# Kernel tuning notes

Hardware: AMD Instinct MI355X
Metric: run time of the kernel (lower is better)

## Reference

```python
import jax, jax.numpy as jnp
import numpy as np

B, S, HID, NH, CACHE = 2, 1024, 1024, 16, 4096
HD = HID // NH
HOT = max(4, CACHE // 4)
COLD = CACHE - HOT
COMP = HID // 2
EPS = 1e-5


def setup_inputs() -> dict:
    key = jax.random.key(0)
    ks = jax.random.split(key, 16)
    std = 0.02
    inp = {
        'inputs': jax.random.normal(ks[0], (B, S, HID), jnp.float32),
        'hot_keys': std * jax.random.normal(ks[1], (HOT, HID), jnp.float32),
        'hot_values': std * jax.random.normal(ks[2], (HOT, HID), jnp.float32),
        'hot_age': jnp.zeros((HOT,), jnp.float32),
        'hot_access': jnp.zeros((HOT,), jnp.float32),
        'cold_keys': std * jax.random.normal(ks[3], (COLD, HID), jnp.float32),
        'cold_values': std * jax.random.normal(ks[4], (COLD, HID), jnp.float32),
        'cold_age': jnp.zeros((COLD,), jnp.float32),
        'cold_access': jnp.zeros((COLD,), jnp.float32),
        # linear weights stored [in, out] (y = x @ W + b)
        'Wq': std * jax.random.normal(ks[5], (HID, HID), jnp.float32),
        'bq': jnp.zeros((HID,), jnp.float32),
        'Wk': std * jax.random.normal(ks[6], (HID, HID), jnp.float32),
        'bk': jnp.zeros((HID,), jnp.float32),
        'Wv': std * jax.random.normal(ks[7], (HID, HID), jnp.float32),
        'bv': jnp.zeros((HID,), jnp.float32),
        'Wo': std * jax.random.normal(ks[8], (HID, HID), jnp.float32),
        'bo': jnp.zeros((HID,), jnp.float32),
        'Wc': (1.0 / np.sqrt(HID)) * jax.random.normal(ks[9], (HID, COMP), jnp.float32),
        'bc': jnp.zeros((COMP,), jnp.float32),
        'Wd': (1.0 / np.sqrt(COMP)) * jax.random.normal(ks[10], (COMP, HID), jnp.float32),
        'bd': jnp.zeros((HID,), jnp.float32),
        'gamma': jnp.ones((HID,), jnp.float32),
        'beta': jnp.zeros((HID,), jnp.float32),
    }
    return inp


def _cache_level(q, cache_k, v_flat, age, access, Wk, bk, Wo, bo):
    # q: [B, NH, S, HD]; cache_k/v_flat: [C, HID]
    C = cache_k.shape[0]
    k = (cache_k @ Wk + bk).reshape(C, NH, HD)
    v = v_flat.reshape(C, NH, HD)
    scores = jnp.einsum('bhsd,chd->bhsc', q, k) / np.sqrt(HD)
    scores = scores + (-0.1 * age + 0.05 * access)  # broadcast over [B,H,S,C]
    attn = jax.nn.softmax(scores, axis=-1)
    out = jnp.einsum('bhsc,chd->bhsd', attn, v)
    out = out.transpose(0, 2, 1, 3).reshape(q.shape[0], q.shape[2], HID)
    return out @ Wo + bo


def reference(inputs, hot_keys, hot_values, hot_age, hot_access,
              cold_keys, cold_values, cold_age, cold_access,
              Wq, bq, Wk, bk, Wv, bv, Wo, bo, Wc, bc, Wd, bd, gamma, beta):
    q = (inputs @ Wq + bq).reshape(B, S, NH, HD).transpose(0, 2, 1, 3)
    # hot tier: values through value_net
    hot_v = hot_values @ Wv + bv
    hot_out = _cache_level(q, hot_keys, hot_v, hot_age, hot_access, Wk, bk, Wo, bo)
    # cold tier: values through compressor -> decompressor
    cold_v = (cold_values @ Wc + bc) @ Wd + bd
    cold_out = _cache_level(q, cold_keys, cold_v, cold_age, cold_access, Wk, bk, Wo, bo)
    x = hot_out + cold_out
    mu = jnp.mean(x, axis=-1, keepdims=True)
    var = jnp.mean(jnp.square(x - mu), axis=-1, keepdims=True)
    return (x - mu) / jnp.sqrt(var + EPS) * gamma + beta
```

## Files before the change

### kernel.cpp

```cpp
#include <hip/hip_runtime.h>

#define BBATCH 2
#define SS   1024
#define HID  1024
#define NH   16
#define HD   64
#define HOT  1024
#define COLD 3072
#define COMP 512

typedef __attribute__((ext_vector_type(8))) short s8v;
typedef __attribute__((ext_vector_type(4))) float f4v;
typedef unsigned short u16;
typedef unsigned int   u32;

__device__ __forceinline__ float b2f(u16 u){ return __uint_as_float(((u32)u)<<16); }
__device__ __forceinline__ u16 f2b(float f){
  u32 u = __float_as_uint(f);
  u += 0x7FFF + ((u>>16)&1);
  return (u16)(u>>16);
}
__device__ __forceinline__ u32 pk2r(u32 a, u32 b){
  return __builtin_amdgcn_perm(b + 0x8000u, a + 0x8000u, 0x07060302u);
}
__device__ __forceinline__ float ldsc(const void* p, int i, int isf32){
  return isf32 ? ((const float*)p)[i] : b2f(((const u16*)p)[i]);
}

__global__ void detect_kernel(const u32* __restrict__ gamma_raw, u32* __restrict__ flag){
  if (threadIdx.x == 0) flag[0] = (gamma_raw[0] == 0x3F800000u) ? 1u : 0u;
}

__global__ __launch_bounds__(256) void bias_kernel(
    const void* __restrict__ h_age, const void* __restrict__ h_acc,
    const void* __restrict__ c_age, const void* __restrict__ c_acc,
    float* __restrict__ BiasH, float* __restrict__ BiasC, const u32* __restrict__ flag)
{
  const int f = (int)flag[0];
  const int i = blockIdx.x * 256 + threadIdx.x;
  if (i < HOT) BiasH[i] = -0.1f * ldsc(h_age, i, f) + 0.05f * ldsc(h_acc, i, f);
  const int j = i - HOT;
  if (j >= 0 && j < COLD) BiasC[j] = -0.1f * ldsc(c_age, j, f) + 0.05f * ldsc(c_acc, j, f);
}

struct TDesc { const void* S; u16* D; int R, C, cshift, tile0; };
struct TBatch { TDesc d[6]; int nd; };

__global__ __launch_bounds__(256) void transpose_kernel(TBatch tb, const u32* __restrict__ flag)
{
  __shared__ __align__(16) u16 Tt[64][72];
  int di = 0;
  for (int i = 1; i < tb.nd; i++) if ((int)blockIdx.x >= tb.d[i].tile0) di = i;
  const TDesc g = tb.d[di];
  const int local = blockIdx.x - g.tile0;
  const int ty = local >> g.cshift;
  const int tx = local & ((1 << g.cshift) - 1);
  const int r0 = ty * 64, c0 = tx * 64;
  const int f = (int)flag[0];
  const int t = threadIdx.x;
  const int sr = t >> 2, sc = (t & 3) * 16;

  union { uint4 q[2]; u16 h[16]; } u;
  if (f) {
    const float* s = (const float*)g.S + (size_t)(r0 + sr) * g.C + c0 + sc;
    const uint4 a = *(const uint4*)s,     b = *(const uint4*)(s + 4);
    const uint4 c = *(const uint4*)(s + 8), d2 = *(const uint4*)(s + 12);
    u.q[0] = (uint4){ pk2r(a.x,a.y), pk2r(a.z,a.w), pk2r(b.x,b.y), pk2r(b.z,b.w) };
    u.q[1] = (uint4){ pk2r(c.x,c.y), pk2r(c.z,c.w), pk2r(d2.x,d2.y), pk2r(d2.z,d2.w) };
  } else {
    const u16* s = (const u16*)g.S + (size_t)(r0 + sr) * g.C + c0 + sc;
    u.q[0] = *(const uint4*)s;  u.q[1] = *(const uint4*)(s + 8);
  }
  #pragma unroll
  for (int i = 0; i < 16; i++) Tt[sc + i][sr] = u.h[i];
  __syncthreads();

  const int dc = t >> 2, dr = (t & 3) * 16;
  const uint4 o0 = *(const uint4*)&Tt[dc][dr];
  const uint4 o1 = *(const uint4*)&Tt[dc][dr + 8];
  u16* dp = g.D + (size_t)(c0 + dc) * g.R + r0 + dr;
  *(uint4*)dp = o0;  *(uint4*)(dp + 8) = o1;
}

#define BM 128
#define BN 128
#define BK 32
struct GemmDesc {
  const void* A; const u16* BT; const void* bias; u16* C;
  int aflag, bcol0, M, N, K, nxlog, tile0, ctrans;
  float bias_scale;
};
struct GemmBatch { GemmDesc d[6]; int nd; };

__global__ __launch_bounds__(256) void gemm_multi(GemmBatch bat, const u32* __restrict__ flag)
{
  __shared__ __align__(16) u16 As[BM][BK + 8];
  __shared__ __align__(16) u16 Bs[BN][BK + 8];

  int di = 0;
  for (int i = 1; i < bat.nd; i++) if ((int)blockIdx.x >= bat.d[i].tile0) di = i;
  const GemmDesc g = bat.d[di];
  const int local = blockIdx.x - g.tile0;
  const int ty = local >> g.nxlog;
  const int tx = local - (ty << g.nxlog);
  const int m0 = ty * BM, n0 = tx * BN;

  const int f  = (int)flag[0];
  const int af = g.aflag ? f : 0;

  const int tid  = threadIdx.x;
  const int lane = tid & 63, wave = tid >> 6;
  const int quad = lane >> 4, l15 = lane & 15;
  const int wm = (wave >> 1) * 64, wn = (wave & 1) * 64;

  f4v acc[4][4];
  #pragma unroll
  for (int i = 0; i < 4; i++)
    #pragma unroll
    for (int j = 0; j < 4; j++) acc[i][j] = (f4v){0.f,0.f,0.f,0.f};

  const int ra = tid >> 1, ka = (tid & 1) * 16;

  uint4 a0, a1, a2, a3;
  uint4 b0, b1;

  auto load_tile = [&](int kk) {
    if (af) {
      const float* s = (const float*)g.A + (size_t)(m0 + ra) * g.K + kk + ka;
      a0 = *(const uint4*)s;      a1 = *(const uint4*)(s + 4);
      a2 = *(const uint4*)(s + 8); a3 = *(const uint4*)(s + 12);
    } else {
      const u16* s = (const u16*)g.A + (size_t)(m0 + ra) * g.K + kk + ka;
      a0 = *(const uint4*)s;  a1 = *(const uint4*)(s + 8);
    }
    const u16* bs = g.BT + (size_t)(g.bcol0 + n0 + ra) * g.K + kk + ka;
    b0 = *(const uint4*)bs;  b1 = *(const uint4*)(bs + 8);
  };

  load_tile(0);

  for (int k0 = 0; k0 < g.K; k0 += BK) {
    __syncthreads();
    if (af) {
      *(uint4*)&As[ra][ka] =
        (uint4){ pk2r(a0.x,a0.y), pk2r(a0.z,a0.w), pk2r(a1.x,a1.y), pk2r(a1.z,a1.w) };
      *(uint4*)&As[ra][ka + 8] =
        (uint4){ pk2r(a2.x,a2.y), pk2r(a2.z,a2.w), pk2r(a3.x,a3.y), pk2r(a3.z,a3.w) };
    } else {
      *(uint4*)&As[ra][ka] = a0;  *(uint4*)&As[ra][ka + 8] = a1;
    }
    *(uint4*)&Bs[ra][ka] = b0;  *(uint4*)&Bs[ra][ka + 8] = b1;
    __syncthreads();

    if (k0 + BK < g.K) load_tile(k0 + BK);

    s8v afr[4], bfr[4];
    #pragma unroll
    for (int i = 0; i < 4; i++)
      afr[i] = *(const s8v*)&As[wm + i * 16 + l15][quad * 8];
    #pragma unroll
    for (int j = 0; j < 4; j++)
      bfr[j] = *(const s8v*)&Bs[wn + j * 16 + l15][quad * 8];

    #pragma unroll
    for (int j = 0; j < 4; j++)
      #pragma unroll
      for (int i = 0; i < 4; i++)
        acc[i][j] = __builtin_amdgcn_mfma_f32_16x16x32_bf16(afr[i], bfr[j], acc[i][j], 0, 0, 0);
  }

  if (g.ctrans) {
    #pragma unroll
    for (int j = 0; j < 4; j++) {
      const int col = n0 + wn + j * 16 + l15;
      const float bv = ldsc(g.bias, g.bcol0 + col, f) * g.bias_scale;
      #pragma unroll
      for (int i = 0; i < 4; i++) {
        const int row = m0 + wm + i * 16 + quad * 4;
        u16 t4[4];
        #pragma unroll
        for (int r = 0; r < 4; r++) t4[r] = f2b(acc[i][j][r] + bv);
        *(uint2*)&g.C[(size_t)col * g.M + row] = *(uint2*)t4;
      }
    }
  } else {
    #pragma unroll
    for (int j = 0; j < 4; j++) {
      const int col = n0 + wn + j * 16 + l15;
      const float bv = ldsc(g.bias, g.bcol0 + col, f) * g.bias_scale;
      #pragma unroll
      for (int i = 0; i < 4; i++) {
        const int row = m0 + wm + i * 16 + quad * 4;
        #pragma unroll
        for (int r = 0; r < 4; r++)
          g.C[(size_t)(row + r) * g.N + col] = f2b(acc[i][j][r] + bv);
      }
    }
  }
}

__global__ __launch_bounds__(256) void attn_kernel(
    const u16* __restrict__ Q,
    const u16* __restrict__ KHg, const u16* __restrict__ VHT,
    const u16* __restrict__ KCg, const u16* __restrict__ VCT,
    const float* __restrict__ BiasH, const float* __restrict__ BiasC,
    float* __restrict__ HotOut, float* __restrict__ ColdNum, float* __restrict__ ColdZ,
    int NG, int glog)
{
  __shared__ __align__(16) u16 Ks[64][72];
  __shared__ __align__(16) u16 Vs[64][72];
  __shared__ __align__(16) u16 Ps[64][72];

  const int tid  = threadIdx.x;
  const int lane = tid & 63, wave = tid >> 6;
  const int quad = lane >> 4, l15 = lane & 15;
  const int bx    = blockIdx.x;
  const int slice = bx & 3;
  const int sblk  = (bx >> 2) & 15;
  const int h     = (bx >> 6) & ((1 << glog) - 1);
  const int b     = bx >> (6 + glog);
  const int rowbase = b * SS + sblk * 64;
  const int hoff  = h * HD;
  const int myrow = wave * 16;

  const bool hot = (slice == 0);
  const u16*  Kt   = hot ? KHg : KCg;
  const u16*  Vt   = hot ? VHT : VCT;
  const float* Bias = hot ? BiasH : BiasC;
  const int   e0  = hot ? 0 : (slice - 1) * 1024;
  const int   ldv = hot ? HOT : COLD;

  const u16* qp = Q + (size_t)(rowbase + myrow + l15) * NG + hoff + quad * 8;
  const s8v aq0 = *(const s8v*)qp;
  const s8v aq1 = *(const s8v*)(qp + 32);

  const int rk = tid >> 2, sk = (tid & 3) * 16;
  const u16* kbase = Kt + (size_t)(e0 + rk) * NG + hoff + sk;
  const u16* vbase = Vt + (size_t)(hoff + rk) * ldv + e0 + sk;
  uint4 kr0 = *(const uint4*)kbase, kr1 = *(const uint4*)(kbase + 8);
  uint4 vr0 = *(const uint4*)vbase, vr1 = *(const uint4*)(vbase + 8);

  f4v o[4];
  #pragma unroll
  for (int j = 0; j < 4; j++) o[j] = (f4v){0.f,0.f,0.f,0.f};
  float z[4] = {0.f,0.f,0.f,0.f};

  for (int c0 = 0; c0 < 1024; c0 += 64) {
    __syncthreads();
    *(uint4*)&Ks[rk][sk] = kr0;  *(uint4*)&Ks[rk][sk + 8] = kr1;
    *(uint4*)&Vs[rk][sk] = vr0;  *(uint4*)&Vs[rk][sk + 8] = vr1;
    __syncthreads();
    if (c0 + 64 < 1024) {
      const u16* kn = kbase + (size_t)(c0 + 64) * NG;
      const u16* vn = vbase + (c0 + 64);
      kr0 = *(const uint4*)kn;  kr1 = *(const uint4*)(kn + 8);
      vr0 = *(const uint4*)vn;  vr1 = *(const uint4*)(vn + 8);
    }

    #pragma unroll
    for (int j = 0; j < 4; j++) {
      f4v s = (f4v){0.f,0.f,0.f,0.f};
      const s8v bk0 = *(const s8v*)&Ks[j * 16 + l15][quad * 8];
      const s8v bk1 = *(const s8v*)&Ks[j * 16 + l15][32 + quad * 8];
      s = __builtin_amdgcn_mfma_f32_16x16x32_bf16(aq0, bk0, s, 0, 0, 0);
      s = __builtin_amdgcn_mfma_f32_16x16x32_bf16(aq1, bk1, s, 0, 0, 0);
      const int cg = e0 + c0 + j * 16 + l15;
      const float bias = Bias[cg];
      #pragma unroll
      for (int r = 0; r < 4; r++) {
        const float ev = __expf(fminf(s[r] * 0.125f + bias, 30.f));
        z[r] += ev;
        Ps[myrow + quad * 4 + r][j * 16 + l15] =
            (u16)((__float_as_uint(ev) + 0x8000u) >> 16);
      }
    }
    const s8v ap0 = *(const s8v*)&Ps[myrow + l15][quad * 8];
    const s8v ap1 = *(const s8v*)&Ps[myrow + l15][32 + quad * 8];
    #pragma unroll
    for (int j = 0; j < 4; j++) {
      const s8v bv0 = *(const s8v*)&Vs[j * 16 + l15][quad * 8];
      const s8v bv1 = *(const s8v*)&Vs[j * 16 + l15][32 + quad * 8];
      o[j] = __builtin_amdgcn_mfma_f32_16x16x32_bf16(ap0, bv0, o[j], 0, 0, 0);
      o[j] = __builtin_amdgcn_mfma_f32_16x16x32_bf16(ap1, bv1, o[j], 0, 0, 0);
    }
  }

  #pragma unroll
  for (int m = 1; m < 16; m <<= 1)
    #pragma unroll
    for (int r = 0; r < 4; r++) z[r] += __shfl_xor(z[r], m, 64);

  if (hot) {
    float rz[4];
    #pragma unroll
    for (int r = 0; r < 4; r++) rz[r] = 1.0f / z[r];
    #pragma unroll
    for (int j = 0; j < 4; j++) {
      const int col = hoff + j * 16 + l15;
      #pragma unroll
      for (int r = 0; r < 4; r++) {
        const int row = rowbase + myrow + quad * 4 + r;
        HotOut[(size_t)row * NG + col] = o[j][r] * rz[r];
      }
    }
  } else {
    #pragma unroll
    for (int j = 0; j < 4; j++) {
      const int col = hoff + j * 16 + l15;
      #pragma unroll
      for (int r = 0; r < 4; r++) {
        const int row = rowbase + myrow + quad * 4 + r;
        atomicAdd(&ColdNum[(size_t)row * NG + col], o[j][r]);
      }
    }
    if (l15 == 0) {
      #pragma unroll
      for (int r = 0; r < 4; r++) {
        const int row = rowbase + myrow + quad * 4 + r;
        atomicAdd(&ColdZ[(size_t)row * (1 << glog) + h], z[r]);
      }
    }
  }
}

__global__ __launch_bounds__(256) void combine_kernel(
    const float* __restrict__ HotOut, float* __restrict__ ColdNum,
    float* __restrict__ ColdZ, u16* __restrict__ ATT,
    int att_ld, int att_c0, int NG, int glog)
{
  const int gid   = blockIdx.x * 256 + threadIdx.x;
  const int shift = 4 + glog;
  const int row   = gid >> shift;
  const int c4    = (gid & ((1 << shift) - 1)) << 2;
  const int h     = c4 >> 6;
  const int G     = 1 << glog;

  const float4 hv = *(const float4*)&HotOut[(size_t)row * NG + c4];
  float4* cp = (float4*)&ColdNum[(size_t)row * NG + c4];
  const float4 cn = *cp;
  const float zi = 1.0f / ColdZ[(size_t)row * G + h];

  u16 ov[4];
  ov[0] = f2b(hv.x + cn.x * zi); ov[1] = f2b(hv.y + cn.y * zi);
  ov[2] = f2b(hv.z + cn.z * zi); ov[3] = f2b(hv.w + cn.w * zi);
  *(uint2*)&ATT[(size_t)row * att_ld + att_c0 + c4] = *(uint2*)ov;

  *cp = (float4){0.f,0.f,0.f,0.f};
  if ((c4 & 63) == 0) ColdZ[(size_t)row * G + h] = 0.f;
}

__global__ __launch_bounds__(256) void ln_kernel(
    const u16* __restrict__ X, const void* __restrict__ gamma,
    const void* __restrict__ beta, void* __restrict__ outp,
    const u32* __restrict__ flag)
{
  __shared__ float red[4];
  const int f = (int)flag[0];
  const int row = blockIdx.x, tid = threadIdx.x;
  const u16* xr = X + (size_t)row * HID;

  float x[4];
  { union { uint2 q; u16 hx[4]; } bx2;
    bx2.q = *(const uint2*)(xr + tid * 4);
    #pragma unroll
    for (int i = 0; i < 4; i++) x[i] = b2f(bx2.hx[i]); }

  float s = x[0] + x[1] + x[2] + x[3];
  #pragma unroll
  for (int m = 1; m < 64; m <<= 1) s += __shfl_xor(s, m, 64);
  if ((tid & 63) == 0) red[tid >> 6] = s;
  __syncthreads();
  const float mu = (red[0] + red[1] + red[2] + red[3]) * (1.0f / HID);
  __syncthreads();

  float v = 0.f;
  #pragma unroll
  for (int i = 0; i < 4; i++) { const float d = x[i] - mu; v += d * d; }
  #pragma unroll
  for (int m = 1; m < 64; m <<= 1) v += __shfl_xor(v, m, 64);
  if ((tid & 63) == 0) red[tid >> 6] = v;
  __syncthreads();
  const float var  = (red[0] + red[1] + red[2] + red[3]) * (1.0f / HID);
  const float rstd = 1.0f / sqrtf(var + 1e-5f);

  #pragma unroll
  for (int i = 0; i < 4; i++) {
    const int col = tid * 4 + i;
    const float val = (x[i] - mu) * rstd * ldsc(gamma, col, f) + ldsc(beta, col, f);
    if (f) ((float*)outp)[(size_t)row * HID + col] = val;
    else   ((u16*) outp)[(size_t)row * HID + col] = f2b(val);
  }
}

extern "C" void kernel_launch(void* const* d_in, const int* in_sizes, int n_in,
                              void* d_out, int out_size, void* d_ws, size_t ws_size,
                              hipStream_t stream)
{
  const void* inputs      = d_in[0];
  const void* hot_keys    = d_in[1];
  const void* hot_values  = d_in[2];
  const void* hot_age     = d_in[3];
  const void* hot_access  = d_in[4];
  const void* cold_keys   = d_in[5];
  const void* cold_values = d_in[6];
  const void* cold_age    = d_in[7];
  const void* cold_access = d_in[8];
  const void* Wq = d_in[9];   const void* bq = d_in[10];
  const void* Wk = d_in[11];  const void* bk = d_in[12];
  const void* Wv = d_in[13];  const void* bv = d_in[14];
  const void* Wo = d_in[15];  const void* bo = d_in[16];
  const void* Wc = d_in[17];  const void* bc = d_in[18];
  const void* Wd = d_in[19];  const void* bd = d_in[20];
  const void* gamma = d_in[21];
  const void* beta  = d_in[22];

  const size_t wtBytes = (size_t)(4 * 1024 * 1024 + 512 * 1024 + 1024 * 512) * 2;
  const size_t xBytes  = (size_t)2048 * HID * 2;
  int G = 0, glog = 0;
  for (int cand = 8, cl = 3; cand >= 2; cand >>= 1, cl--) {
    const int ng = 64 * cand;
    const size_t part = (size_t)2048 * ng * 8 + (size_t)2048 * cand * 4;
    const size_t rpb  = part > xBytes ? part : xBytes;
    const size_t need = 256 + 16384 + wtBytes + rpb + (size_t)10240 * ng * 2;
    if (need <= ws_size) { G = cand; glog = cl; break; }
  }
  if (G == 0) return;
  const int NG = 64 * G;

  char* base = (char*)d_ws;
  u32*  flag  = (u32*)base;
  float* BiasH = (float*)(base + 256);
  float* BiasC = BiasH + HOT;
  u16* WqT = (u16*)(base + 256 + 16384);
  u16* WkT = WqT + (size_t)1024 * 1024;
  u16* WvT = WkT + (size_t)1024 * 1024;
  u16* WoT = WvT + (size_t)1024 * 1024;
  u16* WcT = WoT + (size_t)1024 * 1024;
  u16* WdT = WcT + (size_t)512 * 1024;
  char* rp = (char*)(WdT + (size_t)1024 * 512);
  u16*   X       = (u16*)rp;
  float* HotOut  = (float*)rp;
  float* ColdNum = (float*)(rp + (size_t)2048 * NG * 4);
  float* ColdZ   = (float*)(rp + (size_t)2048 * NG * 8);
  const size_t partBytes = (size_t)2048 * NG * 8 + (size_t)2048 * G * 4;
  const size_t rpBytes   = partBytes > xBytes ? partBytes : xBytes;
  u16* Qg    = (u16*)(rp + rpBytes);
  u16* KHg   = Qg  + (size_t)2048 * NG;
  u16* KCg   = KHg + (size_t)HOT  * NG;
  u16* VHT   = KCg + (size_t)COLD * NG;
  u16* VCT   = VHT + (size_t)HOT  * NG;
  u16* ATT   = (u16*)d_out;
  u16* CVmid = (u16*)d_out + (size_t)2048 * 1024;

  const dim3 blk(256);
  const int nx  = NG >> 7;
  const int nxl = glog - 1;

  const int mQ = 2048 / BM, mH = HOT / BM, mC = COLD / BM;

  detect_kernel<<<dim3(1), dim3(64), 0, stream>>>((const u32*)gamma, flag);
  bias_kernel<<<dim3((HOT + COLD) / 256), blk, 0, stream>>>(
      hot_age, hot_access, cold_age, cold_access, BiasH, BiasC, flag);

  { TBatch tb; tb.nd = 6; int t = 0;
    tb.d[0] = { Wq, WqT, 1024, 1024, 4, t }; t += 256;
    tb.d[1] = { Wk, WkT, 1024, 1024, 4, t }; t += 256;
    tb.d[2] = { Wv, WvT, 1024, 1024, 4, t }; t += 256;
    tb.d[3] = { Wo, WoT, 1024, 1024, 4, t }; t += 256;
    tb.d[4] = { Wc, WcT, 1024,  512, 3, t }; t += 128;
    tb.d[5] = { Wd, WdT,  512, 1024, 4, t }; t += 128;
    transpose_kernel<<<dim3(t), blk, 0, stream>>>(tb, flag);
  }
  hipMemsetAsync(ColdNum, 0, (size_t)2048 * NG * 4 + (size_t)2048 * G * 4, stream);

  { GemmBatch bb; bb.nd = 5; int t = 0;
    bb.d[0] = { inputs,      WqT, bq, Qg,    1, 0, 2048, NG,  1024, nxl, t, 0, 1.0f }; t += nx * mQ;
    bb.d[1] = { hot_keys,    WkT, bk, KHg,   1, 0, HOT,  NG,  1024, nxl, t, 0, 1.0f }; t += nx * mH;
    bb.d[2] = { cold_keys,   WkT, bk, KCg,   1, 0, COLD, NG,  1024, nxl, t, 0, 1.0f }; t += nx * mC;
    bb.d[3] = { hot_values,  WvT, bv, VHT,   1, 0, HOT,  NG,  1024, nxl, t, 1, 1.0f }; t += nx * mH;
    bb.d[4] = { cold_values, WcT, bc, CVmid, 1, 0, COLD, 512, 1024, 2,   t, 0, 1.0f }; t += 4 * mC;
    gemm_multi<<<dim3(t), blk, 0, stream>>>(bb, flag);
  }
  { GemmBatch bb; bb.nd = 1;
    bb.d[0] = { CVmid, WdT, bd, VCT, 0, 0, COLD, NG, 512, nxl, 0, 1, 1.0f };
    gemm_multi<<<dim3(nx * mC), blk, 0, stream>>>(bb, flag);
  }
  attn_kernel<<<dim3(BBATCH * G * 16 * 4), blk, 0, stream>>>(
      Qg, KHg, VHT, KCg, VCT, BiasH, BiasC,
      HotOut, ColdNum, ColdZ, NG, glog);
  combine_kernel<<<dim3((2048 * (NG / 4)) / 256), blk, 0, stream>>>(
      HotOut, ColdNum, ColdZ, ATT, HID, 0, NG, glog);

  for (int p = 1; p < NH / G; ++p) {
    const int c0 = p * NG;
    GemmBatch bb; bb.nd = 5; int t = 0;
    bb.d[0] = { inputs,      WqT, bq, Qg,  1, c0, 2048, NG, 1024, nxl, t, 0, 1.0f }; t += nx * mQ;
    bb.d[1] = { hot_keys,    WkT, bk, KHg, 1, c0, HOT,  NG, 1024, nxl, t, 0, 1.0f }; t += nx * mH;
    bb.d[2] = { cold_keys,   WkT, bk, KCg, 1, c0, COLD, NG, 1024, nxl, t, 0, 1.0f }; t += nx * mC;
    bb.d[3] = { hot_values,  WvT, bv, VHT, 1, c0, HOT,  NG, 1024, nxl, t, 1, 1.0f }; t += nx * mH;
    bb.d[4] = { CVmid,       WdT, bd, VCT, 0, c0, COLD, NG, 512,  nxl, t, 1, 1.0f }; t += nx * mC;
    gemm_multi<<<dim3(t), blk, 0, stream>>>(bb, flag);

    attn_kernel<<<dim3(BBATCH * G * 16 * 4), blk, 0, stream>>>(
        Qg, KHg, VHT, KCg, VCT, BiasH, BiasC,
        HotOut, ColdNum, ColdZ, NG, glog);

    combine_kernel<<<dim3((2048 * (NG / 4)) / 256), blk, 0, stream>>>(
        HotOut, ColdNum, ColdZ, ATT, HID, c0, NG, glog);
  }

  { GemmBatch bb; bb.nd = 1;
    bb.d[0] = { ATT, WoT, bo, X, 0, 0, 2048, 1024, 1024, 3, 0, 0, 2.0f };
    gemm_multi<<<dim3(8 * mQ), blk, 0, stream>>>(bb, flag);
  }
  ln_kernel<<<dim3(2048), blk, 0, stream>>>(X, gamma, beta, d_out, flag);
}
```

Measured before the change: 374.5 us.

## Pre-convert activations to bf16, shrink GEMM N-tile, allow all-heads single pass

Adds a convert kernel that turns the fp32 activation inputs into bf16 once, so the GEMMs no longer re-read and convert fp32 data on every head-group pass. The GEMM N tile drops from 128 to 64, which doubles the block count and halves the B-tile loads and accumulators. The workspace planner now prefers G=16, so all heads go through one projection, attention and combine pass when the workspace is large enough, and it falls back to the old looping scheme otherwise. The cost is extra workspace plus one more kernel launch, and each GEMM block now does less reuse per tile.

```diff
diff --git a/kernel.cpp b/kernel.cpp
--- a/kernel.cpp
+++ b/kernel.cpp
@@ -41,6 +41,26 @@
   if (i < HOT) BiasH[i] = -0.1f * ldsc(h_age, i, f) + 0.05f * ldsc(h_acc, i, f);
   const int j = i - HOT;
   if (j >= 0 && j < COLD) BiasC[j] = -0.1f * ldsc(c_age, j, f) + 0.05f * ldsc(c_acc, j, f);
+}
+
+struct CDesc { const void* S; u16* D; int tile0, pad; };
+struct CBatch { CDesc d[5]; int nd; };
+
+__global__ __launch_bounds__(256) void convert_multi(CBatch cb, const u32* __restrict__ flag)
+{
+  int di = 0;
+  for (int i = 1; i < cb.nd; i++) if ((int)blockIdx.x >= cb.d[i].tile0) di = i;
+  const CDesc g = cb.d[di];
+  const int f = (int)flag[0];
+  const size_t e0 = (size_t)(blockIdx.x - g.tile0) * 2048 + (size_t)threadIdx.x * 8;
+  if (f) {
+    const float* s = (const float*)g.S + e0;
+    const uint4 x = *(const uint4*)s, y = *(const uint4*)(s + 4);
+    *(uint4*)(g.D + e0) =
+      (uint4){ pk2r(x.x,x.y), pk2r(x.z,x.w), pk2r(y.x,y.y), pk2r(y.z,y.w) };
+  } else {
+    *(uint4*)(g.D + e0) = *(const uint4*)((const u16*)g.S + e0);
+  }
 }
 
 struct TDesc { const void* S; u16* D; int R, C, cshift, tile0; };
@@ -83,7 +103,7 @@
 }
 
 #define BM 128
-#define BN 128
+#define BN 64
 #define BK 32
 struct GemmDesc {
   const void* A; const u16* BT; const void* bias; u16* C;
@@ -111,30 +131,31 @@
   const int tid  = threadIdx.x;
   const int lane = tid & 63, wave = tid >> 6;
   const int quad = lane >> 4, l15 = lane & 15;
-  const int wm = (wave >> 1) * 64, wn = (wave & 1) * 64;
-
-  f4v acc[4][4];
+  const int wy = wave >> 1, wx = wave & 1;
+
+  f4v acc[4][2];
   #pragma unroll
   for (int i = 0; i < 4; i++)
     #pragma unroll
-    for (int j = 0; j < 4; j++) acc[i][j] = (f4v){0.f,0.f,0.f,0.f};
-
-  const int ra = tid >> 1, ka = (tid & 1) * 16;
+    for (int j = 0; j < 2; j++) acc[i][j] = (f4v){0.f,0.f,0.f,0.f};
+
+  const int ar = tid >> 1, ac = (tid & 1) * 16;
+  const int br = tid >> 2, bc = (tid & 3) * 8;
 
   uint4 a0, a1, a2, a3;
-  uint4 b0, b1;
+  uint4 b0;
 
   auto load_tile = [&](int kk) {
     if (af) {
-      const float* s = (const float*)g.A + (size_t)(m0 + ra) * g.K + kk + ka;
-      a0 = *(const uint4*)s;      a1 = *(const uint4*)(s + 4);
+      const float* s = (const float*)g.A + (size_t)(m0 + ar) * g.K + kk + ac;
+      a0 = *(const uint4*)s;       a1 = *(const uint4*)(s + 4);
       a2 = *(const uint4*)(s + 8); a3 = *(const uint4*)(s + 12);
     } else {
-      const u16* s = (const u16*)g.A + (size_t)(m0 + ra) * g.K + kk + ka;
+      const u16* s = (const u16*)g.A + (size_t)(m0 + ar) * g.K + kk + ac;
       a0 = *(const uint4*)s;  a1 = *(const uint4*)(s + 8);
     }
-    const u16* bs = g.BT + (size_t)(g.bcol0 + n0 + ra) * g.K + kk + ka;
-    b0 = *(const uint4*)bs;  b1 = *(const uint4*)(bs + 8);
+    const u16* bs = g.BT + (size_t)(g.bcol0 + n0 + br) * g.K + kk + bc;
+    b0 = *(const uint4*)bs;
   };
 
   load_tile(0);
@@ -142,28 +163,28 @@
   for (int k0 = 0; k0 < g.K; k0 += BK) {
     __syncthreads();
     if (af) {
-      *(uint4*)&As[ra][ka] =
+      *(uint4*)&As[ar][ac] =
         (uint4){ pk2r(a0.x,a0.y), pk2r(a0.z,a0.w), pk2r(a1.x,a1.y), pk2r(a1.z,a1.w) };
-      *(uint4*)&As[ra][ka + 8] =
+      *(uint4*)&As[ar][ac + 8] =
         (uint4){ pk2r(a2.x,a2.y), pk2r(a2.z,a2.w), pk2r(a3.x,a3.y), pk2r(a3.z,a3.w) };
     } else {
-      *(uint4*)&As[ra][ka] = a0;  *(uint4*)&As[ra][ka + 8] = a1;
-    }
-    *(uint4*)&Bs[ra][ka] = b0;  *(uint4*)&Bs[ra][ka + 8] = b1;
+      *(uint4*)&As[ar][ac] = a0;  *(uint4*)&As[ar][ac + 8] = a1;
+    }
+    *(uint4*)&Bs[br][bc] = b0;
     __syncthreads();
 
     if (k0 + BK < g.K) load_tile(k0 + BK);
 
-    s8v afr[4], bfr[4];
+    s8v afr[4], bfr[2];
     #pragma unroll
     for (int i = 0; i < 4; i++)
-      afr[i] = *(const s8v*)&As[wm + i * 16 + l15][quad * 8];
-    #pragma unroll
-    for (int j = 0; j < 4; j++)
-      bfr[j] = *(const s8v*)&Bs[wn + j * 16 + l15][quad * 8];
-
-    #pragma unroll
-    for (int j = 0; j < 4; j++)
+      afr[i] = *(const s8v*)&As[wy * 64 + i * 16 + l15][quad * 8];
+    #pragma unroll
+    for (int j = 0; j < 2; j++)
+      bfr[j] = *(const s8v*)&Bs[wx * 32 + j * 16 + l15][quad * 8];
+
+    #pragma unroll
+    for (int j = 0; j < 2; j++)
       #pragma unroll
       for (int i = 0; i < 4; i++)
         acc[i][j] = __builtin_amdgcn_mfma_f32_16x16x32_bf16(afr[i], bfr[j], acc[i][j], 0, 0, 0);
@@ -171,12 +192,12 @@
 
   if (g.ctrans) {
     #pragma unroll
-    for (int j = 0; j < 4; j++) {
-      const int col = n0 + wn + j * 16 + l15;
+    for (int j = 0; j < 2; j++) {
+      const int col = n0 + wx * 32 + j * 16 + l15;
       const float bv = ldsc(g.bias, g.bcol0 + col, f) * g.bias_scale;
       #pragma unroll
       for (int i = 0; i < 4; i++) {
-        const int row = m0 + wm + i * 16 + quad * 4;
+        const int row = m0 + wy * 64 + i * 16 + quad * 4;
         u16 t4[4];
         #pragma unroll
         for (int r = 0; r < 4; r++) t4[r] = f2b(acc[i][j][r] + bv);
@@ -185,12 +206,12 @@
     }
   } else {
     #pragma unroll
-    for (int j = 0; j < 4; j++) {
-      const int col = n0 + wn + j * 16 + l15;
+    for (int j = 0; j < 2; j++) {
+      const int col = n0 + wx * 32 + j * 16 + l15;
       const float bv = ldsc(g.bias, g.bcol0 + col, f) * g.bias_scale;
       #pragma unroll
       for (int i = 0; i < 4; i++) {
-        const int row = m0 + wm + i * 16 + quad * 4;
+        const int row = m0 + wy * 64 + i * 16 + quad * 4;
         #pragma unroll
         for (int r = 0; r < 4; r++)
           g.C[(size_t)(row + r) * g.N + col] = f2b(acc[i][j][r] + bv);
@@ -414,54 +435,82 @@
   const void* gamma = d_in[21];
   const void* beta  = d_in[22];
 
-  const size_t wtBytes = (size_t)(4 * 1024 * 1024 + 512 * 1024 + 1024 * 512) * 2;
-  const size_t xBytes  = (size_t)2048 * HID * 2;
-  int G = 0, glog = 0;
-  for (int cand = 8, cl = 3; cand >= 2; cand >>= 1, cl--) {
-    const int ng = 64 * cand;
-    const size_t part = (size_t)2048 * ng * 8 + (size_t)2048 * cand * 4;
-    const size_t rpb  = part > xBytes ? part : xBytes;
-    const size_t need = 256 + 16384 + wtBytes + rpb + (size_t)10240 * ng * 2;
-    if (need <= ws_size) { G = cand; glog = cl; break; }
-  }
-  if (G == 0) return;
+  const size_t FIX    = 256 + 16384;
+  const size_t WT     = (size_t)10 * 1024 * 1024;
+  const size_t COPIES = (size_t)10240 * 1024 * 2;
+  const size_t XB     = (size_t)2048 * HID * 2;
+  auto PART = [](int Gc){ return (size_t)2048 * (64 * Gc) * 8 + (size_t)2048 * Gc * 4; };
+  auto BUFS = [](int Gc){ return (size_t)10240 * (64 * Gc) * 2; };
+  auto MX   = [](size_t a, size_t b){ return a > b ? a : b; };
+
+  int G = 0, docopy = 0;
+  { const size_t needF = FIX + WT + MX(COPIES, MX(PART(16), XB)) + BUFS(16);
+    if (ws_size >= needF) { G = 16; docopy = 1; } }
+  for (int c = 8; c >= 2 && !G; c >>= 1)
+    if (ws_size >= FIX + WT + COPIES + MX(PART(c), XB) + BUFS(c)) { G = c; docopy = 1; }
+  for (int c = 8; c >= 2 && !G; c >>= 1)
+    if (ws_size >= FIX + WT + MX(PART(c), XB) + BUFS(c)) { G = c; docopy = 0; }
+  if (!G) return;
+  const int glog = (G == 16) ? 4 : (G == 8 ? 3 : (G == 4 ? 2 : 1));
   const int NG = 64 * G;
-
-  char* base = (char*)d_ws;
+  const bool full = (G == 16);
+
+  char* base  = (char*)d_ws;
   u32*  flag  = (u32*)base;
   float* BiasH = (float*)(base + 256);
   float* BiasC = BiasH + HOT;
-  u16* WqT = (u16*)(base + 256 + 16384);
+  u16* WqT = (u16*)(base + FIX);
   u16* WkT = WqT + (size_t)1024 * 1024;
   u16* WvT = WkT + (size_t)1024 * 1024;
   u16* WoT = WvT + (size_t)1024 * 1024;
   u16* WcT = WoT + (size_t)1024 * 1024;
   u16* WdT = WcT + (size_t)512 * 1024;
-  char* rp = (char*)(WdT + (size_t)1024 * 512);
+  char* rp0 = base + FIX + WT;
+
+  u16* inputsB = (u16*)rp0;
+  u16* hotkB   = inputsB + (size_t)2048 * 1024;
+  u16* coldkB  = hotkB   + (size_t)1024 * 1024;
+  u16* hotvB   = coldkB  + (size_t)3072 * 1024;
+  u16* coldvB  = hotvB   + (size_t)1024 * 1024;
+
+  char* rp = rp0 + ((docopy && !full) ? COPIES : 0);
   u16*   X       = (u16*)rp;
   float* HotOut  = (float*)rp;
   float* ColdNum = (float*)(rp + (size_t)2048 * NG * 4);
   float* ColdZ   = (float*)(rp + (size_t)2048 * NG * 8);
-  const size_t partBytes = (size_t)2048 * NG * 8 + (size_t)2048 * G * 4;
-  const size_t rpBytes   = partBytes > xBytes ? partBytes : xBytes;
-  u16* Qg    = (u16*)(rp + rpBytes);
-  u16* KHg   = Qg  + (size_t)2048 * NG;
-  u16* KCg   = KHg + (size_t)HOT  * NG;
-  u16* VHT   = KCg + (size_t)COLD * NG;
-  u16* VCT   = VHT + (size_t)HOT  * NG;
+  const size_t Rbytes = full ? MX(COPIES, MX(PART(16), XB)) : MX(PART(G), XB);
+  u16* Qg  = (u16*)(rp + Rbytes);
+  u16* KHg = Qg  + (size_t)2048 * NG;
+  u16* KCg = KHg + (size_t)HOT  * NG;
+  u16* VHT = KCg + (size_t)COLD * NG;
+  u16* VCT = VHT + (size_t)HOT  * NG;
   u16* ATT   = (u16*)d_out;
   u16* CVmid = (u16*)d_out + (size_t)2048 * 1024;
 
+  const void* Aq = docopy ? (const void*)inputsB : inputs;
+  const void* Ahk = docopy ? (const void*)hotkB  : hot_keys;
+  const void* Ack = docopy ? (const void*)coldkB : cold_keys;
+  const void* Ahv = docopy ? (const void*)hotvB  : hot_values;
+  const void* Acv = docopy ? (const void*)coldvB : cold_values;
+  const int afl = docopy ? 0 : 1;
+
   const dim3 blk(256);
-  const int nx  = NG >> 7;
-  const int nxl = glog - 1;
-
   const int mQ = 2048 / BM, mH = HOT / BM, mC = COLD / BM;
+  const size_t coldPart = (size_t)2048 * NG * 4 + (size_t)2048 * G * 4;
 
   detect_kernel<<<dim3(1), dim3(64), 0, stream>>>((const u32*)gamma, flag);
   bias_kernel<<<dim3((HOT + COLD) / 256), blk, 0, stream>>>(
       hot_age, hot_access, cold_age, cold_access, BiasH, BiasC, flag);
 
+  if (docopy) {
+    CBatch cb; cb.nd = 5; int t = 0;
+    cb.d[0] = { inputs,      inputsB, t, 0 }; t += 1024;
+    cb.d[1] = { hot_keys,    hotkB,   t, 0 }; t += 512;
+    cb.d[2] = { cold_keys,   coldkB,  t, 0 }; t += 1536;
+    cb.d[3] = { hot_values,  hotvB,   t, 0 }; t += 512;
+    cb.d[4] = { cold_values, coldvB,  t, 0 }; t += 1536;
+    convert_multi<<<dim3(t), blk, 0, stream>>>(cb, flag);
+  }
   { TBatch tb; tb.nd = 6; int t = 0;
     tb.d[0] = { Wq, WqT, 1024, 1024, 4, t }; t += 256;
     tb.d[1] = { Wk, WkT, 1024, 1024, 4, t }; t += 256;
@@ -471,47 +520,64 @@
     tb.d[5] = { Wd, WdT,  512, 1024, 4, t }; t += 128;
     transpose_kernel<<<dim3(t), blk, 0, stream>>>(tb, flag);
   }
-  hipMemsetAsync(ColdNum, 0, (size_t)2048 * NG * 4 + (size_t)2048 * G * 4, stream);
-
-  { GemmBatch bb; bb.nd = 5; int t = 0;
-    bb.d[0] = { inputs,      WqT, bq, Qg,    1, 0, 2048, NG,  1024, nxl, t, 0, 1.0f }; t += nx * mQ;
-    bb.d[1] = { hot_keys,    WkT, bk, KHg,   1, 0, HOT,  NG,  1024, nxl, t, 0, 1.0f }; t += nx * mH;
-    bb.d[2] = { cold_keys,   WkT, bk, KCg,   1, 0, COLD, NG,  1024, nxl, t, 0, 1.0f }; t += nx * mC;
-    bb.d[3] = { hot_values,  WvT, bv, VHT,   1, 0, HOT,  NG,  1024, nxl, t, 1, 1.0f }; t += nx * mH;
-    bb.d[4] = { cold_values, WcT, bc, CVmid, 1, 0, COLD, 512, 1024, 2,   t, 0, 1.0f }; t += 4 * mC;
-    gemm_multi<<<dim3(t), blk, 0, stream>>>(bb, flag);
-  }
+
+  if (full) {
+    { GemmBatch bb; bb.nd = 5; int t = 0;
+      bb.d[0] = { Aq,  WqT, bq, Qg,    afl, 0, 2048, 1024, 1024, 4, t, 0, 1.0f }; t += 16 * mQ;
+      bb.d[1] = { Ahk, WkT, bk, KHg,   afl, 0, HOT,  1024, 1024, 4, t, 0, 1.0f }; t += 16 * mH;
+      bb.d[2] = { Ack, WkT, bk, KCg,   afl, 0, COLD, 1024, 1024, 4, t, 0, 1.0f }; t += 16 * mC;
+      bb.d[3] = { Ahv, WvT, bv, VHT,   afl, 0, HOT,  1024, 1024, 4, t, 1, 1.0f }; t += 16 * mH;
+      bb.d[4] = { Acv, WcT, bc, CVmid, afl, 0, COLD,  512, 1024, 3, t, 0, 1.0f }; t += 8 * mC;
+      gemm_multi<<<dim3(t), blk, 0, stream>>>(bb, flag);
+    }
+    { GemmBatch bb; bb.nd = 1;
+      bb.d[0] = { CVmid, WdT, bd, VCT, 0, 0, COLD, 1024, 512, 4, 0, 1, 1.0f };
+      gemm_multi<<<dim3(16 * mC), blk, 0, stream>>>(bb, flag);
+    }
+    hipMemsetAsync(ColdNum, 0, coldPart, stream);
+    attn_kernel<<<dim3(BBATCH * 16 * 16 * 4), blk, 0, stream>>>(
+        Qg, KHg, VHT, KCg, VCT, BiasH, BiasC, HotOut, ColdNum, ColdZ, NG, glog);
+    combine_kernel<<<dim3((2048 * (NG / 4)) / 256), blk, 0, stream>>>(
+        HotOut, ColdNum, ColdZ, ATT, HID, 0, NG, glog);
+  } else {
+    hipMemsetAsync(ColdNum, 0, coldPart, stream);
+    { GemmBatch bb; bb.nd = 5; int t = 0;
+      bb.d[0] = { Aq,  WqT, bq, Qg,    afl, 0, 2048, NG,  1024, glog, t, 0, 1.0f }; t += G * mQ;
+      bb.d[1] = { Ahk, WkT, bk, KHg,   afl, 0, HOT,  NG,  1024, glog, t, 0, 1.0f }; t += G * mH;
+      bb.d[2] = { Ack, WkT, bk, KCg,   afl, 0, COLD, NG,  1024, glog, t, 0, 1.0f }; t += G * mC;
+      bb.d[3] = { Ahv, WvT, bv, VHT,   afl, 0, HOT,  NG,  1024, glog, t, 1, 1.0f }; t += G * mH;
+      bb.d[4] = { Acv, WcT, bc, CVmid, afl, 0, COLD, 512, 1024, 3,    t, 0, 1.0f }; t += 8 * mC;
+      gemm_multi<<<dim3(t), blk, 0, stream>>>(bb, flag);
+    }
+    { GemmBatch bb; bb.nd = 1;
+      bb.d[0] = { CVmid, WdT, bd, VCT, 0, 0, COLD, NG, 512, glog, 0, 1, 1.0f };
+      gemm_multi<<<dim3(G * mC), blk, 0, stream>>>(bb, flag);
+    }
+    attn_kernel<<<dim3(BBATCH * G * 16 * 4), blk, 0, stream>>>(
+        Qg, KHg, VHT, KCg, VCT, BiasH, BiasC, HotOut, ColdNum, ColdZ, NG, glog);
+    combine_kernel<<<dim3((2048 * (NG / 4)) / 256), blk, 0, stream>>>(
+        HotOut, ColdNum, ColdZ, ATT, HID, 0, NG, glog);
+
+    for (int p = 1; p < NH / G; ++p) {
+      const int c0 = p * NG;
+      GemmBatch bb; bb.nd = 5; int t = 0;
+      bb.d[0] = { Aq,    WqT, bq, Qg,  afl, c0, 2048, NG, 1024, glog, t, 0, 1.0f }; t += G * mQ;
+      bb.d[1] = { Ahk,   WkT, bk, KHg, afl, c0, HOT,  NG, 1024, glog, t, 0, 1.0f }; t += G * mH;
+      bb.d[2] = { Ack,   WkT, bk, KCg, afl, c0, COLD, NG, 1024, glog, t, 0, 1.0f }; t += G * mC;
+      bb.d[3] = { Ahv,   WvT, bv, VHT, afl, c0, HOT,  NG, 1024, glog, t, 1, 1.0f }; t += G * mH;
+      bb.d[4] = { CVmid, WdT, bd, VCT, 0,   c0, COLD, NG, 512,  glog, t, 1, 1.0f }; t += G * mC;
+      gemm_multi<<<dim3(t), blk, 0, stream>>>(bb, flag);
+
+      attn_kernel<<<dim3(BBATCH * G * 16 * 4), blk, 0, stream>>>(
+          Qg, KHg, VHT, KCg, VCT, BiasH, BiasC, HotOut, ColdNum, ColdZ, NG, glog);
+      combine_kernel<<<dim3((2048 * (NG / 4)) / 256), blk, 0, stream>>>(
+          HotOut, ColdNum, ColdZ, ATT, HID, c0, NG, glog);
+    }
+  }
+
   { GemmBatch bb; bb.nd = 1;
-    bb.d[0] = { CVmid, WdT, bd, VCT, 0, 0, COLD, NG, 512, nxl, 0, 1, 1.0f };
-    gemm_multi<<<dim3(nx * mC), blk, 0, stream>>>(bb, flag);
-  }
-  attn_kernel<<<dim3(BBATCH * G * 16 * 4), blk, 0, stream>>>(
-      Qg, KHg, VHT, KCg, VCT, BiasH, BiasC,
-      HotOut, ColdNum, ColdZ, NG, glog);
-  combine_kernel<<<dim3((2048 * (NG / 4)) / 256), blk, 0, stream>>>(
-      HotOut, ColdNum, ColdZ, ATT, HID, 0, NG, glog);
-
-  for (int p = 1; p < NH / G; ++p) {
-    const int c0 = p * NG;
-    GemmBatch bb; bb.nd = 5; int t = 0;
-    bb.d[0] = { inputs,      WqT, bq, Qg,  1, c0, 2048, NG, 1024, nxl, t, 0, 1.0f }; t += nx * mQ;
-    bb.d[1] = { hot_keys,    WkT, bk, KHg, 1, c0, HOT,  NG, 1024, nxl, t, 0, 1.0f }; t += nx * mH;
-    bb.d[2] = { cold_keys,   WkT, bk, KCg, 1, c0, COLD, NG, 1024, nxl, t, 0, 1.0f }; t += nx * mC;
-    bb.d[3] = { hot_values,  WvT, bv, VHT, 1, c0, HOT,  NG, 1024, nxl, t, 1, 1.0f }; t += nx * mH;
-    bb.d[4] = { CVmid,       WdT, bd, VCT, 0, c0, COLD, NG, 512,  nxl, t, 1, 1.0f }; t += nx * mC;
-    gemm_multi<<<dim3(t), blk, 0, stream>>>(bb, flag);
-
-    attn_kernel<<<dim3(BBATCH * G * 16 * 4), blk, 0, stream>>>(
-        Qg, KHg, VHT, KCg, VCT, BiasH, BiasC,
-        HotOut, ColdNum, ColdZ, NG, glog);
-
-    combine_kernel<<<dim3((2048 * (NG / 4)) / 256), blk, 0, stream>>>(
-        HotOut, ColdNum, ColdZ, ATT, HID, c0, NG, glog);
-  }
-
-  { GemmBatch bb; bb.nd = 1;
-    bb.d[0] = { ATT, WoT, bo, X, 0, 0, 2048, 1024, 1024, 3, 0, 0, 2.0f };
-    gemm_multi<<<dim3(8 * mQ), blk, 0, stream>>>(bb, flag);
+    bb.d[0] = { ATT, WoT, bo, X, 0, 0, 2048, 1024, 1024, 4, 0, 0, 2.0f };
+    gemm_multi<<<dim3(16 * mQ), blk, 0, stream>>>(bb, flag);
   }
   ln_kernel<<<dim3(2048), blk, 0, stream>>>(X, gamma, beta, d_out, flag);
 }
```

Result: faster. 320.0 us (-14.5%).
